# Optimization experiments

Measured on AMD Instinct MI355X. Metric: run time of the kernel, lower is better.

## Reference

```python
import jax, jax.numpy as jnp
import numpy as np
from jax import lax

DN = ('NCHW', 'OIHW', 'NCHW')

def conv(x, w, pad='VALID'):
    return lax.conv_general_dilated(x, w, (1, 1), pad, dimension_numbers=DN)

def adaptive_matrix(in_s, out_s):
    # exact torch adaptive_avg_pool2d bin weights: start=floor(i*in/out), end=ceil((i+1)*in/out)
    M = np.zeros((out_s, in_s), np.float32)
    for i in range(out_s):
        s = (i * in_s) // out_s
        e = -(-((i + 1) * in_s) // out_s)
        M[i, s:e] = 1.0 / (e - s)
    return jnp.asarray(M)

def setup_inputs() -> dict:
    key = jax.random.key(0)
    ks = jax.random.split(key, 11)
    C = 64
    def w(k, shape, fan_in):
        return jax.random.normal(k, shape, jnp.float32) * (1.0 / np.sqrt(fan_in))
    return {
        'x': jax.random.normal(ks[0], (16, C, 128, 128), jnp.float32),
        'conv1_w': w(ks[1], (2 * C, C, 1, 1), C),
        'conv1_b': jnp.zeros((2 * C,), jnp.float32),
        'conv2_w': w(ks[2], (C, C, 1, 1), C),
        'conv2_b': jnp.zeros((C,), jnp.float32),
        'conv3_w': w(ks[3], (C, 2 * C, 1, 1), 2 * C),
        'conv3_b': jnp.zeros((C,), jnp.float32),
        'pos_w': w(ks[4], (C, C, 3, 3), C * 9),
        'pos_b': jnp.zeros((C,), jnp.float32),
        'se_w1': w(ks[5], (C // 8, C, 1, 1), C),
        'se_w2': w(ks[6], (C, C // 8, 1, 1), C // 8),
    }

def reference(x, conv1_w, conv1_b, conv2_w, conv2_b, conv3_w, conv3_b, pos_w, pos_b, se_w1, se_w2):
    C, nw, ext = 64, 4, 4
    y = conv(x, conv1_w) + conv1_b[None, :, None, None]
    x1, x2 = y[:, :C], y[:, C:]
    N, _, H, W = x1.shape
    x1p = jnp.pad(x1, ((0, 0), (0, 0), (ext, ext), (ext, ext)), mode='edge')
    Hp, Wp = H + 2 * ext, W + 2 * ext
    Hs, Ws = H // nw, W // nw
    Hk, Wk = Hs + H % nw, Ws + W % nw
    Hps, Wps = Hp // nw, Wp // nw
    Hpk, Wpk = Hps + Hp % nw, Wps + Wp % nw
    # unfold: windows row-major (h_window fastest over j), shape (N, nw^2, C, Hpk, Wpk)
    wins = jnp.stack([x1p[:, :, i * Hps:i * Hps + Hpk, j * Wps:j * Wps + Wpk]
                      for i in range(nw) for j in range(nw)], axis=1)
    Ph = adaptive_matrix(Hpk, Hk)
    Pw = adaptive_matrix(Wpk, Wk)
    pooled = jnp.einsum('nlchw,Hh,Ww->nlcHW', wins, Ph, Pw).reshape(N * nw * nw, C, Hk, Wk)
    pr = (conv(pooled, conv2_w) + conv2_b[None, :, None, None]
          + conv(pooled, pos_w, 'SAME') + pos_b[None, :, None, None])
    # SE attention
    s = jnp.mean(pr, axis=(2, 3), keepdims=True)
    s = jax.nn.sigmoid(conv(jax.nn.relu(conv(s, se_w1)), se_w2))
    att = pr * s + pr
    # faithful torch .view(N, C*Hk*Wk, nw^2) memory reinterpretation, then fold
    cols = att.reshape(N, nw * nw * C * Hk * Wk).reshape(N, C, Hk, Wk, nw * nw)
    out = jnp.zeros((N, C, H, W), x.dtype)
    cnt = jnp.zeros((N, 1, H, W), x.dtype)
    for i in range(nw):
        for j in range(nw):
            l = i * nw + j
            out = out.at[:, :, i * Hs:i * Hs + Hk, j * Ws:j * Ws + Wk].add(cols[..., l])
            cnt = cnt.at[:, :, i * Hs:i * Hs + Hk, j * Ws:j * Ws + Wk].add(1.0)
    out = out / cnt
    return conv(jnp.concatenate([out, x2], axis=1), conv3_w) + conv3_b[None, :, None, None]
```

## Files before the change

### kernel.cpp

```cpp
#include <hip/hip_runtime.h>

constexpr int N = 16, C = 64, H = 128, W = 128, P = H * W;
constexpr int NL = 256, PK = 1024;

constexpr size_t OFF_RA    = 0;
constexpr size_t OFF_RB    = 8388608;
constexpr size_t OFF_RC    = 16777216;
constexpr size_t OFF_SUMS  = 25165824;
constexpr size_t OFF_SCALE = OFF_SUMS  + 16384;
constexpr size_t OFF_WMOD  = OFF_SCALE + 16384;
constexpr size_t OFF_W1L   = OFF_WMOD  + 18432;
constexpr size_t OFF_W3L   = OFF_W1L   + 4096;

typedef short bf16x8 __attribute__((ext_vector_type(8)));
typedef float f32x4  __attribute__((ext_vector_type(4)));

__device__ inline unsigned short f2bf(float f) {
    unsigned u = __float_as_uint(f);
    unsigned r = (u + 0x7FFFu + ((u >> 16) & 1u)) >> 16;
    return (unsigned short)r;
}
__device__ inline float bf2f(unsigned short h) {
    return __uint_as_float(((unsigned)h) << 16);
}

__global__ __launch_bounds__(256) void k0_prep(const float* __restrict__ pos_w,
                                               const float* __restrict__ conv2_w,
                                               const float* __restrict__ w1,
                                               const float* __restrict__ w3,
                                               unsigned short* __restrict__ wmod,
                                               unsigned short* __restrict__ w1lay,
                                               unsigned short* __restrict__ w3lay,
                                               float* __restrict__ sums) {
    int t = blockIdx.x * 256 + threadIdx.x;
    if (t < 36864) {
        int cir = t & 31;
        int co  = (t >> 5) & 63;
        int cib = (t >> 11) & 1;
        int tap = t >> 12;
        int ci  = cib * 32 + cir;
        float v = pos_w[(co * 64 + ci) * 9 + tap];
        if (tap == 4) v += conv2_w[co * 64 + ci];
        wmod[t] = f2bf(v);
    } else if (t < 45056) {
        int u = t - 36864;
        int cir = u & 31;
        int co  = (u >> 5) & 127;
        int cib = u >> 12;
        w1lay[u] = f2bf(w1[co * 64 + cib * 32 + cir]);
    } else if (t < 53248) {
        int u = t - 45056;
        int cir = u & 31;
        int co  = (u >> 5) & 63;
        int cib = u >> 11;
        w3lay[u] = f2bf(w3[co * 128 + cib * 32 + cir]);
    } else {
        sums[t - 53248] = 0.f;
    }
}

__global__ __launch_bounds__(256) void k1_conv1(const float* __restrict__ x,
                                                const unsigned short* __restrict__ w1lay,
                                                const float* __restrict__ b1,
                                                unsigned short* __restrict__ x1t,
                                                unsigned short* __restrict__ x2t) {
    int bid = blockIdx.x;
    int n   = bid >> 7;
    int px0 = (bid & 127) << 7;
    int t   = threadIdx.x;
    int wave = t >> 6, lane = t & 63;
    int quad = lane >> 4, l16 = lane & 15;
    int pxw = wave * 32;
    const float* xb = x + (size_t)n * 64 * P + px0 + pxw + l16;
    bf16x8 bfr[2][2];
    #pragma unroll
    for (int cib = 0; cib < 2; ++cib) {
        #pragma unroll
        for (int pt = 0; pt < 2; ++pt) {
            unsigned short tmp[8];
            #pragma unroll
            for (int q = 0; q < 8; ++q)
                tmp[q] = f2bf(xb[(size_t)(cib * 32 + quad * 8 + q) * P + pt * 16]);
            bfr[cib][pt] = *(const bf16x8*)tmp;
        }
    }
    f32x4 acc[8][2] = {};
    #pragma unroll
    for (int cib = 0; cib < 2; ++cib) {
        bf16x8 af[8];
        #pragma unroll
        for (int ct = 0; ct < 8; ++ct)
            af[ct] = *(const bf16x8*)(w1lay + ((size_t)(cib * 128 + ct * 16 + l16)) * 32 + quad * 8);
        #pragma unroll
        for (int ct = 0; ct < 8; ++ct)
            #pragma unroll
            for (int pt = 0; pt < 2; ++pt)
                acc[ct][pt] = __builtin_amdgcn_mfma_f32_16x16x32_bf16(af[ct], bfr[cib][pt], acc[ct][pt], 0, 0, 0);
    }
    #pragma unroll
    for (int ct = 0; ct < 8; ++ct) {
        int co0 = ct * 16 + quad * 4;
        float4 bb = *(const float4*)(b1 + co0);
        #pragma unroll
        for (int pt = 0; pt < 2; ++pt) {
            int px = px0 + pxw + pt * 16 + l16;
            ushort4 o;
            o.x = f2bf(acc[ct][pt][0] + bb.x);
            o.y = f2bf(acc[ct][pt][1] + bb.y);
            o.z = f2bf(acc[ct][pt][2] + bb.z);
            o.w = f2bf(acc[ct][pt][3] + bb.w);
            if (co0 < 64)
                *(ushort4*)(x1t + ((size_t)n * P + px) * 64 + co0) = o;
            else
                *(ushort4*)(x2t + ((size_t)n * P + px) * 64 + (co0 - 64)) = o;
        }
    }
}

__global__ __launch_bounds__(256) void k3_pool_pr(const unsigned short* __restrict__ x1t,
                                                  const unsigned short* __restrict__ wmod,
                                                  const float* __restrict__ b2,
                                                  const float* __restrict__ posb,
                                                  unsigned short* __restrict__ prb,
                                                  float* __restrict__ sums) {
    __shared__ __align__(16) unsigned short lxs[340 * 64];
    int bid = blockIdx.x;
    int nl  = bid >> 2;
    int r0  = (bid & 3) * 8;
    int n   = nl >> 4, wl = nl & 15;
    int wi  = wl >> 2, wj = wl & 3;
    int t   = threadIdx.x;
    const unsigned short* xb = x1t + (size_t)n * P * 64;
    for (int it = 0; it < 11; ++it) {
        int e = t + it * 256;
        if (e < 2720) {
            int pix = e >> 3, part = e & 7;
            int lr = pix / 34, lc = pix - lr * 34;
            int gr = r0 - 1 + lr, gc = lc - 1;
            unsigned short oc[8];
            if ((unsigned)gr < 32u && (unsigned)gc < 32u) {
                int sh = gr + (gr >> 4), sw = gc + (gc >> 4);
                int u = wi * 34 + sh - 4, v = wj * 34 + sw - 4;
                int ra = min(max(u, 0), 127), rb = min(max(u + 1, 0), 127);
                int ca = min(max(v, 0), 127), cb = min(max(v + 1, 0), 127);
                int off = part * 8;
                uint4 A = *(const uint4*)(xb + (size_t)(ra * 128 + ca) * 64 + off);
                uint4 B = *(const uint4*)(xb + (size_t)(ra * 128 + cb) * 64 + off);
                uint4 Cc = *(const uint4*)(xb + (size_t)(rb * 128 + ca) * 64 + off);
                uint4 D = *(const uint4*)(xb + (size_t)(rb * 128 + cb) * 64 + off);
                const unsigned short* a = (const unsigned short*)&A;
                const unsigned short* b = (const unsigned short*)&B;
                const unsigned short* c = (const unsigned short*)&Cc;
                const unsigned short* d = (const unsigned short*)&D;
                #pragma unroll
                for (int q = 0; q < 8; ++q)
                    oc[q] = f2bf(0.25f * (bf2f(a[q]) + bf2f(b[q]) + bf2f(c[q]) + bf2f(d[q])));
            } else {
                #pragma unroll
                for (int q = 0; q < 8; ++q) oc[q] = 0;
            }
            *(uint4*)(lxs + pix * 64 + ((part ^ (pix & 7)) * 8)) = *(const uint4*)oc;
        }
    }
    __syncthreads();
    int wave = t >> 6, lane = t & 63;
    int quad = lane >> 4, l16 = lane & 15;
    int wrow0 = wave * 2;
    f32x4 acc[4][4] = {};
    #pragma unroll
    for (int cib = 0; cib < 2; ++cib) {
        #pragma unroll
        for (int tap = 0; tap < 9; ++tap) {
            int dh = tap / 3, dw = tap % 3;
            bf16x8 af[4], bfr[4];
            #pragma unroll
            for (int ct = 0; ct < 4; ++ct)
                af[ct] = *(const bf16x8*)(wmod + (((tap * 2 + cib) * 64) + ct * 16 + l16) * 32 + quad * 8);
            #pragma unroll
            for (int pt = 0; pt < 4; ++pt) {
                int pix = (wrow0 + (pt >> 1) + dh) * 34 + ((pt & 1) * 16 + l16 + dw);
                int chunk = cib * 4 + quad;
                bfr[pt] = *(const bf16x8*)(lxs + pix * 64 + ((chunk ^ (pix & 7)) * 8));
            }
            #pragma unroll
            for (int ct = 0; ct < 4; ++ct)
                #pragma unroll
                for (int pt = 0; pt < 4; ++pt)
                    acc[ct][pt] = __builtin_amdgcn_mfma_f32_16x16x32_bf16(af[ct], bfr[pt], acc[ct][pt], 0, 0, 0);
        }
    }
    #pragma unroll
    for (int ct = 0; ct < 4; ++ct) {
        #pragma unroll
        for (int r = 0; r < 4; ++r) {
            int co = ct * 16 + quad * 4 + r;
            float bias = b2[co] + posb[co];
            float s = 0.f;
            #pragma unroll
            for (int pt = 0; pt < 4; ++pt) {
                float v = acc[ct][pt][r] + bias;
                int row = r0 + wrow0 + (pt >> 1);
                int col = (pt & 1) * 16 + l16;
                prb[(size_t)nl * 65536 + co * 1024 + row * 32 + col] = f2bf(v);
                s += v;
            }
            s += __shfl_xor(s, 1);
            s += __shfl_xor(s, 2);
            s += __shfl_xor(s, 4);
            s += __shfl_xor(s, 8);
            if (l16 == 0) atomicAdd(&sums[nl * 64 + co], s);
        }
    }
}

__global__ __launch_bounds__(64) void k3b_se(const float* __restrict__ sums,
                                             const float* __restrict__ w1,
                                             const float* __restrict__ w2,
                                             float* __restrict__ scale) {
    __shared__ float m[64];
    __shared__ float hid[8];
    int nl = blockIdx.x;
    int t  = threadIdx.x;
    m[t] = sums[nl * 64 + t] * (1.f / 1024.f);
    __syncthreads();
    if (t < 8) {
        float s = 0.f;
        #pragma unroll
        for (int ci = 0; ci < 64; ++ci) s += w1[t * 64 + ci] * m[ci];
        hid[t] = fmaxf(s, 0.f);
    }
    __syncthreads();
    float v = 0.f;
    #pragma unroll
    for (int r = 0; r < 8; ++r) v += w2[t * 8 + r] * hid[r];
    scale[nl * 64 + t] = 1.f + 1.f / (1.f + __expf(-v));
}

__global__ __launch_bounds__(256) void k5_conv3(const unsigned short* __restrict__ prb,
                                                const float* __restrict__ scale,
                                                const unsigned short* __restrict__ x2t,
                                                const unsigned short* __restrict__ w3lay,
                                                const float* __restrict__ b3,
                                                float* __restrict__ out) {
    __shared__ __align__(16) unsigned short lxs[128 * 136];
    int bid = blockIdx.x;
    int n   = bid >> 7;
    int row = bid & 127;
    int i   = row >> 5, h2 = row & 31;
    int px0 = row << 7;
    int t   = threadIdx.x;
    const unsigned short* src2 = x2t + ((size_t)n * P + (size_t)row * 128) * 64;
    #pragma unroll
    for (int it = 0; it < 4; ++it) {
        int e = t + it * 256;
        int pix = e >> 3, part = e & 7;
        *(uint4*)(lxs + pix * 136 + 64 + part * 8) = *(const uint4*)(src2 + pix * 64 + part * 8);
    }
    int c2 = t >> 5, w2 = t & 31;
    int cc_b = h2 >> 1;
    int hb = (h2 & 1) * 512 + w2 * 16 + i * 4;
    #pragma unroll
    for (int mm = 0; mm < 2; ++mm) {
        int nl = n * 16 + c2 * 2 + mm;
        const unsigned short* pb = prb + (size_t)nl * 65536 + (size_t)cc_b * 1024 + hb;
        const float* sb = scale + nl * 64 + cc_b;
        ushort4 v0 = *(const ushort4*)(pb);
        ushort4 v1 = *(const ushort4*)(pb + 16 * 1024);
        ushort4 v2 = *(const ushort4*)(pb + 32 * 1024);
        ushort4 v3 = *(const ushort4*)(pb + 48 * 1024);
        float s0 = sb[0], s1 = sb[16], s2 = sb[32], s3 = sb[48];
        unsigned short* d = lxs + w2 * 136 + c2 * 8 + mm * 4;
        ushort4 o;
        o.x = f2bf(bf2f(v0.x) * s0); o.y = f2bf(bf2f(v1.x) * s1);
        o.z = f2bf(bf2f(v2.x) * s2); o.w = f2bf(bf2f(v3.x) * s3);
        *(ushort4*)(d) = o;
        o.x = f2bf(bf2f(v0.y) * s0); o.y = f2bf(bf2f(v1.y) * s1);
        o.z = f2bf(bf2f(v2.y) * s2); o.w = f2bf(bf2f(v3.y) * s3);
        *(ushort4*)(d + 32 * 136) = o;
        o.x = f2bf(bf2f(v0.z) * s0); o.y = f2bf(bf2f(v1.z) * s1);
        o.z = f2bf(bf2f(v2.z) * s2); o.w = f2bf(bf2f(v3.z) * s3);
        *(ushort4*)(d + 64 * 136) = o;
        o.x = f2bf(bf2f(v0.w) * s0); o.y = f2bf(bf2f(v1.w) * s1);
        o.z = f2bf(bf2f(v2.w) * s2); o.w = f2bf(bf2f(v3.w) * s3);
        *(ushort4*)(d + 96 * 136) = o;
    }
    __syncthreads();
    int wave = t >> 6, lane = t & 63;
    int quad = lane >> 4, l16 = lane & 15;
    int pxw = wave * 32;
    f32x4 acc[4][2] = {};
    #pragma unroll
    for (int cib = 0; cib < 4; ++cib) {
        bf16x8 af[4], bfr[2];
        #pragma unroll
        for (int ct = 0; ct < 4; ++ct)
            af[ct] = *(const bf16x8*)(w3lay + ((size_t)(cib * 64 + ct * 16 + l16)) * 32 + quad * 8);
        #pragma unroll
        for (int pt = 0; pt < 2; ++pt)
            bfr[pt] = *(const bf16x8*)(lxs + (pxw + pt * 16 + l16) * 136 + cib * 32 + quad * 8);
        #pragma unroll
        for (int ct = 0; ct < 4; ++ct)
            #pragma unroll
            for (int pt = 0; pt < 2; ++pt)
                acc[ct][pt] = __builtin_amdgcn_mfma_f32_16x16x32_bf16(af[ct], bfr[pt], acc[ct][pt], 0, 0, 0);
    }
    #pragma unroll
    for (int ct = 0; ct < 4; ++ct) {
        int co0 = ct * 16 + quad * 4;
        float4 bb = *(const float4*)(b3 + co0);
        #pragma unroll
        for (int pt = 0; pt < 2; ++pt) {
            int px = px0 + pxw + pt * 16 + l16;
            const float* bp = (const float*)&bb;
            #pragma unroll
            for (int r = 0; r < 4; ++r)
                out[((size_t)n * 64 + co0 + r) * P + px] = acc[ct][pt][r] + bp[r];
        }
    }
}

extern "C" void kernel_launch(void* const* d_in, const int* in_sizes, int n_in,
                              void* d_out, int out_size, void* d_ws, size_t ws_size,
                              hipStream_t stream) {
    const float* x       = (const float*)d_in[0];
    const float* conv1_w = (const float*)d_in[1];
    const float* conv1_b = (const float*)d_in[2];
    const float* conv2_w = (const float*)d_in[3];
    const float* conv2_b = (const float*)d_in[4];
    const float* conv3_w = (const float*)d_in[5];
    const float* conv3_b = (const float*)d_in[6];
    const float* pos_w   = (const float*)d_in[7];
    const float* pos_b   = (const float*)d_in[8];
    const float* se_w1   = (const float*)d_in[9];
    const float* se_w2   = (const float*)d_in[10];

    float* ws = (float*)d_ws;
    unsigned short* prb  = (unsigned short*)(ws + OFF_RA);
    unsigned short* x1t  = (unsigned short*)(ws + OFF_RB);
    unsigned short* x2t  = (unsigned short*)(ws + OFF_RC);
    float* sums  = ws + OFF_SUMS;
    float* scale = ws + OFF_SCALE;
    unsigned short* wmod  = (unsigned short*)(ws + OFF_WMOD);
    unsigned short* w1lay = (unsigned short*)(ws + OFF_W1L);
    unsigned short* w3lay = (unsigned short*)(ws + OFF_W3L);

    k0_prep   <<<272,  256, 0, stream>>>(pos_w, conv2_w, conv1_w, conv3_w,
                                         wmod, w1lay, w3lay, sums);
    k1_conv1  <<<2048, 256, 0, stream>>>(x, w1lay, conv1_b, x1t, x2t);
    k3_pool_pr<<<1024, 256, 0, stream>>>(x1t, wmod, conv2_b, pos_b, prb, sums);
    k3b_se    <<<256,  64,  0, stream>>>(sums, se_w1, se_w2, scale);
    k5_conv3  <<<2048, 256, 0, stream>>>(prb, scale, x2t, w3lay, conv3_b, (float*)d_out);
}
```

Baseline: 235.5 us.

## Halve pool/pos-conv tile height, remap blocks, and rewrite SE with wave shuffles

```diff
diff --git a/kernel.cpp b/kernel.cpp
--- a/kernel.cpp
+++ b/kernel.cpp
@@ -123,69 +123,68 @@
                                                   const float* __restrict__ posb,
                                                   unsigned short* __restrict__ prb,
                                                   float* __restrict__ sums) {
-    __shared__ __align__(16) unsigned short lxs[340 * 64];
-    int bid = blockIdx.x;
-    int nl  = bid >> 2;
-    int r0  = (bid & 3) * 8;
+    __shared__ __align__(16) unsigned short lxs[204 * 64];
+    int b   = blockIdx.x;
+    int nl  = (b & 7) | ((b >> 6) << 3);
+    int rc  = (b >> 3) & 7;
+    int r0  = rc * 4;
     int n   = nl >> 4, wl = nl & 15;
     int wi  = wl >> 2, wj = wl & 3;
     int t   = threadIdx.x;
     const unsigned short* xb = x1t + (size_t)n * P * 64;
-    for (int it = 0; it < 11; ++it) {
+    #pragma unroll
+    for (int it = 0; it < 7; ++it) {
         int e = t + it * 256;
-        if (e < 2720) {
+        if (it < 6 || e < 1632) {
             int pix = e >> 3, part = e & 7;
             int lr = pix / 34, lc = pix - lr * 34;
             int gr = r0 - 1 + lr, gc = lc - 1;
+            float mfac = (((unsigned)gr < 32u) && ((unsigned)gc < 32u)) ? 0.25f : 0.f;
+            int grc = min(max(gr, 0), 31), gcc = min(max(gc, 0), 31);
+            int sh = grc + (grc >> 4), sw = gcc + (gcc >> 4);
+            int u = wi * 34 + sh - 4, v = wj * 34 + sw - 4;
+            int ra = min(max(u, 0), 127), rb = min(max(u + 1, 0), 127);
+            int ca = min(max(v, 0), 127), cb = min(max(v + 1, 0), 127);
+            int off = part * 8;
+            uint4 A = *(const uint4*)(xb + (size_t)(ra * 128 + ca) * 64 + off);
+            uint4 B = *(const uint4*)(xb + (size_t)(ra * 128 + cb) * 64 + off);
+            uint4 Cc = *(const uint4*)(xb + (size_t)(rb * 128 + ca) * 64 + off);
+            uint4 D = *(const uint4*)(xb + (size_t)(rb * 128 + cb) * 64 + off);
+            const unsigned short* a = (const unsigned short*)&A;
+            const unsigned short* bb = (const unsigned short*)&B;
+            const unsigned short* c = (const unsigned short*)&Cc;
+            const unsigned short* d = (const unsigned short*)&D;
             unsigned short oc[8];
-            if ((unsigned)gr < 32u && (unsigned)gc < 32u) {
-                int sh = gr + (gr >> 4), sw = gc + (gc >> 4);
-                int u = wi * 34 + sh - 4, v = wj * 34 + sw - 4;
-                int ra = min(max(u, 0), 127), rb = min(max(u + 1, 0), 127);
-                int ca = min(max(v, 0), 127), cb = min(max(v + 1, 0), 127);
-                int off = part * 8;
-                uint4 A = *(const uint4*)(xb + (size_t)(ra * 128 + ca) * 64 + off);
-                uint4 B = *(const uint4*)(xb + (size_t)(ra * 128 + cb) * 64 + off);
-                uint4 Cc = *(const uint4*)(xb + (size_t)(rb * 128 + ca) * 64 + off);
-                uint4 D = *(const uint4*)(xb + (size_t)(rb * 128 + cb) * 64 + off);
-                const unsigned short* a = (const unsigned short*)&A;
-                const unsigned short* b = (const unsigned short*)&B;
-                const unsigned short* c = (const unsigned short*)&Cc;
-                const unsigned short* d = (const unsigned short*)&D;
-                #pragma unroll
-                for (int q = 0; q < 8; ++q)
-                    oc[q] = f2bf(0.25f * (bf2f(a[q]) + bf2f(b[q]) + bf2f(c[q]) + bf2f(d[q])));
-            } else {
-                #pragma unroll
-                for (int q = 0; q < 8; ++q) oc[q] = 0;
-            }
+            #pragma unroll
+            for (int q = 0; q < 8; ++q)
+                oc[q] = f2bf(mfac * (bf2f(a[q]) + bf2f(bb[q]) + bf2f(c[q]) + bf2f(d[q])));
             *(uint4*)(lxs + pix * 64 + ((part ^ (pix & 7)) * 8)) = *(const uint4*)oc;
         }
     }
     __syncthreads();
     int wave = t >> 6, lane = t & 63;
     int quad = lane >> 4, l16 = lane & 15;
-    int wrow0 = wave * 2;
-    f32x4 acc[4][4] = {};
+    int wrow0 = wave;
+    f32x4 acc[4][2] = {};
     #pragma unroll
     for (int cib = 0; cib < 2; ++cib) {
         #pragma unroll
         for (int tap = 0; tap < 9; ++tap) {
             int dh = tap / 3, dw = tap % 3;
-            bf16x8 af[4], bfr[4];
+            bf16x8 af[4], bfr[2];
             #pragma unroll
             for (int ct = 0; ct < 4; ++ct)
                 af[ct] = *(const bf16x8*)(wmod + (((tap * 2 + cib) * 64) + ct * 16 + l16) * 32 + quad * 8);
             #pragma unroll
-            for (int pt = 0; pt < 4; ++pt) {
-                int pix = (wrow0 + (pt >> 1) + dh) * 34 + ((pt & 1) * 16 + l16 + dw);
+            for (int pt = 0; pt < 2; ++pt) {
+                int pix = (wrow0 + dh) * 34 + (pt * 16 + l16 + dw);
                 int chunk = cib * 4 + quad;
                 bfr[pt] = *(const bf16x8*)(lxs + pix * 64 + ((chunk ^ (pix & 7)) * 8));
             }
             #pragma unroll
             for (int ct = 0; ct < 4; ++ct)
                 #pragma unroll
-                for (int pt = 0; pt < 4; ++pt)
+                for (int pt = 0; pt < 2; ++pt)
                     acc[ct][pt] = __builtin_amdgcn_mfma_f32_16x16x32_bf16(af[ct], bfr[pt], acc[ct][pt], 0, 0, 0);
         }
     }
@@ -197,10 +196,10 @@
             float bias = b2[co] + posb[co];
             float s = 0.f;
             #pragma unroll
-            for (int pt = 0; pt < 4; ++pt) {
+            for (int pt = 0; pt < 2; ++pt) {
                 float v = acc[ct][pt][r] + bias;
-                int row = r0 + wrow0 + (pt >> 1);
-                int col = (pt & 1) * 16 + l16;
+                int row = r0 + wrow0;
+                int col = pt * 16 + l16;
                 prb[(size_t)nl * 65536 + co * 1024 + row * 32 + col] = f2bf(v);
                 s += v;
             }
@@ -213,27 +212,29 @@
     }
 }
 
-__global__ __launch_bounds__(64) void k3b_se(const float* __restrict__ sums,
-                                             const float* __restrict__ w1,
-                                             const float* __restrict__ w2,
-                                             float* __restrict__ scale) {
-    __shared__ float m[64];
-    __shared__ float hid[8];
-    int nl = blockIdx.x;
-    int t  = threadIdx.x;
-    m[t] = sums[nl * 64 + t] * (1.f / 1024.f);
-    __syncthreads();
-    if (t < 8) {
-        float s = 0.f;
-        #pragma unroll
-        for (int ci = 0; ci < 64; ++ci) s += w1[t * 64 + ci] * m[ci];
-        hid[t] = fmaxf(s, 0.f);
-    }
-    __syncthreads();
+__global__ __launch_bounds__(256) void k3b_se(const float* __restrict__ sums,
+                                              const float* __restrict__ w1,
+                                              const float* __restrict__ w2,
+                                              float* __restrict__ scale) {
+    int wv   = (blockIdx.x << 2) + (threadIdx.x >> 6);
+    int lane = threadIdx.x & 63;
+    float m = sums[wv * 64 + lane] * (1.f / 1024.f);
+    int h = lane >> 3, sub = lane & 7;
+    float p = 0.f;
+    #pragma unroll
+    for (int k = 0; k < 8; ++k) {
+        int ci = sub * 8 + k;
+        p += w1[h * 64 + ci] * __shfl(m, ci);
+    }
+    p += __shfl_xor(p, 1);
+    p += __shfl_xor(p, 2);
+    p += __shfl_xor(p, 4);
+    float hid = fmaxf(p, 0.f);
     float v = 0.f;
     #pragma unroll
-    for (int r = 0; r < 8; ++r) v += w2[t * 8 + r] * hid[r];
-    scale[nl * 64 + t] = 1.f + 1.f / (1.f + __expf(-v));
+    for (int r = 0; r < 8; ++r)
+        v += w2[lane * 8 + r] * __shfl(hid, r * 8);
+    scale[wv * 64 + lane] = 1.f + 1.f / (1.f + __expf(-v));
 }
 
 __global__ __launch_bounds__(256) void k5_conv3(const unsigned short* __restrict__ prb,
@@ -347,7 +348,7 @@
     k0_prep   <<<272,  256, 0, stream>>>(pos_w, conv2_w, conv1_w, conv3_w,
                                          wmod, w1lay, w3lay, sums);
     k1_conv1  <<<2048, 256, 0, stream>>>(x, w1lay, conv1_b, x1t, x2t);
-    k3_pool_pr<<<1024, 256, 0, stream>>>(x1t, wmod, conv2_b, pos_b, prb, sums);
-    k3b_se    <<<256,  64,  0, stream>>>(sums, se_w1, se_w2, scale);
+    k3_pool_pr<<<2048, 256, 0, stream>>>(x1t, wmod, conv2_b, pos_b, prb, sums);
+    k3b_se    <<<64,   256, 0, stream>>>(sums, se_w1, se_w2, scale);
     k5_conv3  <<<2048, 256, 0, stream>>>(prb, scale, x2t, w3lay, conv3_b, (float*)d_out);
 }
```

After: 250.0 us. 6.2% more time.

## Split pooled input staging by channel half and stage conv weights in LDS

Applied to the files above, without the earlier changes.

```diff
diff --git a/kernel.cpp b/kernel.cpp
--- a/kernel.cpp
+++ b/kernel.cpp
@@ -123,7 +123,8 @@
                                                   const float* __restrict__ posb,
                                                   unsigned short* __restrict__ prb,
                                                   float* __restrict__ sums) {
-    __shared__ __align__(16) unsigned short lxs[340 * 64];
+    __shared__ __align__(16) unsigned short lxs[340 * 32];
+    __shared__ __align__(16) unsigned short lwm[9 * 64 * 32];
     int bid = blockIdx.x;
     int nl  = bid >> 2;
     int r0  = (bid & 3) * 8;
@@ -131,56 +132,66 @@
     int wi  = wl >> 2, wj = wl & 3;
     int t   = threadIdx.x;
     const unsigned short* xb = x1t + (size_t)n * P * 64;
-    for (int it = 0; it < 11; ++it) {
-        int e = t + it * 256;
-        if (e < 2720) {
-            int pix = e >> 3, part = e & 7;
-            int lr = pix / 34, lc = pix - lr * 34;
-            int gr = r0 - 1 + lr, gc = lc - 1;
-            unsigned short oc[8];
-            if ((unsigned)gr < 32u && (unsigned)gc < 32u) {
-                int sh = gr + (gr >> 4), sw = gc + (gc >> 4);
-                int u = wi * 34 + sh - 4, v = wj * 34 + sw - 4;
-                int ra = min(max(u, 0), 127), rb = min(max(u + 1, 0), 127);
-                int ca = min(max(v, 0), 127), cb = min(max(v + 1, 0), 127);
-                int off = part * 8;
-                uint4 A = *(const uint4*)(xb + (size_t)(ra * 128 + ca) * 64 + off);
-                uint4 B = *(const uint4*)(xb + (size_t)(ra * 128 + cb) * 64 + off);
-                uint4 Cc = *(const uint4*)(xb + (size_t)(rb * 128 + ca) * 64 + off);
-                uint4 D = *(const uint4*)(xb + (size_t)(rb * 128 + cb) * 64 + off);
-                const unsigned short* a = (const unsigned short*)&A;
-                const unsigned short* b = (const unsigned short*)&B;
-                const unsigned short* c = (const unsigned short*)&Cc;
-                const unsigned short* d = (const unsigned short*)&D;
-                #pragma unroll
-                for (int q = 0; q < 8; ++q)
-                    oc[q] = f2bf(0.25f * (bf2f(a[q]) + bf2f(b[q]) + bf2f(c[q]) + bf2f(d[q])));
-            } else {
-                #pragma unroll
-                for (int q = 0; q < 8; ++q) oc[q] = 0;
-            }
-            *(uint4*)(lxs + pix * 64 + ((part ^ (pix & 7)) * 8)) = *(const uint4*)oc;
-        }
-    }
-    __syncthreads();
     int wave = t >> 6, lane = t & 63;
     int quad = lane >> 4, l16 = lane & 15;
     int wrow0 = wave * 2;
     f32x4 acc[4][4] = {};
     #pragma unroll
     for (int cib = 0; cib < 2; ++cib) {
+        if (cib) __syncthreads();
+        for (int it = 0; it < 6; ++it) {
+            int e = t + it * 256;
+            if (e < 1360) {
+                int pix = e >> 2, part = e & 3;
+                int lr = pix / 34, lc = pix - lr * 34;
+                int gr = r0 - 1 + lr, gc = lc - 1;
+                unsigned short oc[8];
+                if ((unsigned)gr < 32u && (unsigned)gc < 32u) {
+                    int sh = gr + (gr >> 4), sw = gc + (gc >> 4);
+                    int u = wi * 34 + sh - 4, v = wj * 34 + sw - 4;
+                    int ra = min(max(u, 0), 127), rb = min(max(u + 1, 0), 127);
+                    int ca = min(max(v, 0), 127), cb = min(max(v + 1, 0), 127);
+                    int off = cib * 32 + part * 8;
+                    uint4 A = *(const uint4*)(xb + (size_t)(ra * 128 + ca) * 64 + off);
+                    uint4 B = *(const uint4*)(xb + (size_t)(ra * 128 + cb) * 64 + off);
+                    uint4 Cc = *(const uint4*)(xb + (size_t)(rb * 128 + ca) * 64 + off);
+                    uint4 D = *(const uint4*)(xb + (size_t)(rb * 128 + cb) * 64 + off);
+                    const unsigned short* a = (const unsigned short*)&A;
+                    const unsigned short* b = (const unsigned short*)&B;
+                    const unsigned short* c = (const unsigned short*)&Cc;
+                    const unsigned short* d = (const unsigned short*)&D;
+                    #pragma unroll
+                    for (int q = 0; q < 8; ++q)
+                        oc[q] = f2bf(0.25f * (bf2f(a[q]) + bf2f(b[q]) + bf2f(c[q]) + bf2f(d[q])));
+                } else {
+                    #pragma unroll
+                    for (int q = 0; q < 8; ++q) oc[q] = 0;
+                }
+                *(uint4*)(lxs + pix * 32 + ((part ^ ((pix >> 1) & 3)) * 8)) = *(const uint4*)oc;
+            }
+        }
+        #pragma unroll
+        for (int it = 0; it < 9; ++it) {
+            int e = t + it * 256;
+            int tap = e >> 8, rem = e & 255;
+            int co = rem >> 2, part = rem & 3;
+            *(uint4*)(lwm + (tap * 64 + co) * 32 + ((part ^ ((co >> 1) & 3)) * 8)) =
+                *(const uint4*)(wmod + (((size_t)(tap * 2 + cib) * 64 + co) * 32) + part * 8);
+        }
+        __syncthreads();
         #pragma unroll
         for (int tap = 0; tap < 9; ++tap) {
             int dh = tap / 3, dw = tap % 3;
             bf16x8 af[4], bfr[4];
             #pragma unroll
-            for (int ct = 0; ct < 4; ++ct)
-                af[ct] = *(const bf16x8*)(wmod + (((tap * 2 + cib) * 64) + ct * 16 + l16) * 32 + quad * 8);
+            for (int ct = 0; ct < 4; ++ct) {
+                int co = ct * 16 + l16;
+                af[ct] = *(const bf16x8*)(lwm + (tap * 64 + co) * 32 + ((quad ^ ((co >> 1) & 3)) * 8));
+            }
             #pragma unroll
             for (int pt = 0; pt < 4; ++pt) {
                 int pix = (wrow0 + (pt >> 1) + dh) * 34 + ((pt & 1) * 16 + l16 + dw);
-                int chunk = cib * 4 + quad;
-                bfr[pt] = *(const bf16x8*)(lxs + pix * 64 + ((chunk ^ (pix & 7)) * 8));
+                bfr[pt] = *(const bf16x8*)(lxs + pix * 32 + ((quad ^ ((pix >> 1) & 3)) * 8));
             }
             #pragma unroll
             for (int ct = 0; ct < 4; ++ct)
@@ -213,27 +224,29 @@
     }
 }
 
-__global__ __launch_bounds__(64) void k3b_se(const float* __restrict__ sums,
-                                             const float* __restrict__ w1,
-                                             const float* __restrict__ w2,
-                                             float* __restrict__ scale) {
-    __shared__ float m[64];
-    __shared__ float hid[8];
-    int nl = blockIdx.x;
-    int t  = threadIdx.x;
-    m[t] = sums[nl * 64 + t] * (1.f / 1024.f);
-    __syncthreads();
-    if (t < 8) {
-        float s = 0.f;
-        #pragma unroll
-        for (int ci = 0; ci < 64; ++ci) s += w1[t * 64 + ci] * m[ci];
-        hid[t] = fmaxf(s, 0.f);
-    }
-    __syncthreads();
+__global__ __launch_bounds__(256) void k3b_se(const float* __restrict__ sums,
+                                              const float* __restrict__ w1,
+                                              const float* __restrict__ w2,
+                                              float* __restrict__ scale) {
+    int wv   = (blockIdx.x << 2) + (threadIdx.x >> 6);
+    int lane = threadIdx.x & 63;
+    float m = sums[wv * 64 + lane] * (1.f / 1024.f);
+    int h = lane >> 3, sub = lane & 7;
+    float p = 0.f;
+    #pragma unroll
+    for (int k = 0; k < 8; ++k) {
+        int ci = sub * 8 + k;
+        p += w1[h * 64 + ci] * __shfl(m, ci);
+    }
+    p += __shfl_xor(p, 1);
+    p += __shfl_xor(p, 2);
+    p += __shfl_xor(p, 4);
+    float hid = fmaxf(p, 0.f);
     float v = 0.f;
     #pragma unroll
-    for (int r = 0; r < 8; ++r) v += w2[t * 8 + r] * hid[r];
-    scale[nl * 64 + t] = 1.f + 1.f / (1.f + __expf(-v));
+    for (int r = 0; r < 8; ++r)
+        v += w2[lane * 8 + r] * __shfl(hid, r * 8);
+    scale[wv * 64 + lane] = 1.f + 1.f / (1.f + __expf(-v));
 }
 
 __global__ __launch_bounds__(256) void k5_conv3(const unsigned short* __restrict__ prb,
@@ -348,6 +361,6 @@
                                          wmod, w1lay, w3lay, sums);
     k1_conv1  <<<2048, 256, 0, stream>>>(x, w1lay, conv1_b, x1t, x2t);
     k3_pool_pr<<<1024, 256, 0, stream>>>(x1t, wmod, conv2_b, pos_b, prb, sums);
-    k3b_se    <<<256,  64,  0, stream>>>(sums, se_w1, se_w2, scale);
+    k3b_se    <<<64,   256, 0, stream>>>(sums, se_w1, se_w2, scale);
     k5_conv3  <<<2048, 256, 0, stream>>>(prb, scale, x2t, w3lay, conv3_b, (float*)d_out);
 }
```

Measured after the change: 226.3 us. 3.9% less time.
